# Kernel tuning notes

Measured on AMD Instinct MI355X. Metric: run time of the kernel, lower is better.

The kernel has to match this reference:

```python
import math
import jax, jax.numpy as jnp
import numpy as np

N_HEAD = 16
ROPE_BASE = 10000.0


def _rope_tables(T, half, dtype):
    # build_sin_cos(seq_len, dim=head_dim//2): inv freq of length `half`
    pos = jnp.arange(T, dtype=jnp.float32)[:, None]                       # (T,1)
    inv = jnp.exp(jnp.arange(0, 2 * half, 2, dtype=jnp.float32) * (-math.log(ROPE_BASE) / (2 * half)))
    ang = pos * inv                                                        # (T, half)
    return jnp.sin(ang).astype(dtype), jnp.cos(ang).astype(dtype)


def _apply_rope(q, k, sin, cos):
    # q,k: (B,T,H,Dh); sin,cos: (T, Dh//2) -> broadcast over batch and heads
    half = q.shape[-1] // 2
    s = sin[None, :, None, :]
    c = cos[None, :, None, :]
    q1, q2 = q[..., :half], q[..., half:]
    k1, k2 = k[..., :half], k[..., half:]
    q = jnp.concatenate([q1 * c - q2 * s, q2 * c + q1 * s], axis=-1)
    k = jnp.concatenate([k1 * c - k2 * s, k2 * c + k1 * s], axis=-1)
    return q, k


def setup_inputs() -> dict:
    key = jax.random.key(0)
    k1, k2, k3 = jax.random.split(key, 3)
    B, T, C = 2, 2048, 2048
    x = jax.random.normal(k1, (B, T, C), dtype=jnp.float32)
    w_qkv = jax.random.normal(k2, (3 * C, C), dtype=jnp.float32) * (1.0 / math.sqrt(C))
    w_proj = jax.random.normal(k3, (C, C), dtype=jnp.float32) * (1.0 / math.sqrt(C))
    return {"x": x, "w_qkv": w_qkv, "w_proj": w_proj}


def reference(x, w_qkv, w_proj):
    B, T, C = x.shape
    H = N_HEAD
    Dh = C // H
    # fused QKV projection (Linear, no bias): (B,T,3C) -> (B,T,3,H,Dh)
    qkv = jnp.einsum('btc,oc->bto', x, w_qkv).reshape(B, T, 3, H, Dh)
    q, k, v = qkv[:, :, 0], qkv[:, :, 1], qkv[:, :, 2]          # (B,T,H,Dh)
    sin, cos = _rope_tables(T, Dh // 2, x.dtype)
    q, k = _apply_rope(q, k, sin, cos)
    # causal attention, scale 1/sqrt(Dh) (flash default softmax_scale=None)
    scale = 1.0 / math.sqrt(Dh)
    scores = jnp.einsum('bqhd,bkhd->bhqk', q, k) * scale        # (B,H,T,T)
    mask = jnp.tril(jnp.ones((T, T), dtype=bool))
    scores = jnp.where(mask[None, None], scores, jnp.finfo(scores.dtype).min)
    probs = jax.nn.softmax(scores, axis=-1)
    out = jnp.einsum('bhqk,bkhd->bqhd', probs, v)               # (B,T,H,Dh)
    # faithful to original: permute(0,2,1,3) then reshape_as(x)
    out = jnp.transpose(out, (0, 2, 1, 3)).reshape(B, T, C)
    return jnp.einsum('btc,oc->bto', out, w_proj)
```

## Files before the change

### kernel.cpp

```cpp
#include <hip/hip_runtime.h>
#include <hip/hip_bf16.h>

typedef __bf16 bf16_t;
typedef __bf16 bf16x8 __attribute__((ext_vector_type(8)));
typedef __bf16 bf16x4 __attribute__((ext_vector_type(4)));
typedef float f32x4 __attribute__((ext_vector_type(4)));
typedef float f32x16 __attribute__((ext_vector_type(16)));
typedef unsigned u32x4v __attribute__((ext_vector_type(4)));

#define MFMA16(a, b, c) __builtin_amdgcn_mfma_f32_16x16x32_bf16(a, b, c, 0, 0, 0)
#define MFMA32(a, b, c) __builtin_amdgcn_mfma_f32_32x32x16_bf16(a, b, c, 0, 0, 0)

__device__ __forceinline__ void async_copy16(const void* g, void* l) {
  __builtin_amdgcn_global_load_lds(
      (const __attribute__((address_space(1))) void*)g,
      (__attribute__((address_space(3))) void*)l, 16, 0, 0);
}

__device__ __forceinline__ unsigned cvtpk(float lo, float hi) {
  unsigned r;
  asm("v_cvt_pk_bf16_f32 %0, %1, %2" : "=v"(r) : "v"(lo), "v"(hi));
  return r;
}

__global__ void cast_all(const float* __restrict__ x, const float* __restrict__ wqkv,
                         const float* __restrict__ wproj, bf16_t* __restrict__ xb,
                         bf16_t* __restrict__ wqkvb, bf16_t* __restrict__ wprojb) {
  int stride = gridDim.x * blockDim.x;
  for (int i = blockIdx.x * blockDim.x + threadIdx.x; i < 3145728; i += stride) {
    const float* src;
    bf16_t* dst;
    int idx;
    if (i < 1048576) { src = x; dst = xb; idx = i; }
    else if (i < 2621440) { src = wqkv; dst = wqkvb; idx = i - 1048576; }
    else { src = wproj; dst = wprojb; idx = i - 2621440; }
    const float* p = src + (size_t)idx * 8;
    f32x4 a = *(const f32x4*)p;
    f32x4 b = *(const f32x4*)(p + 4);
    bf16x8 o;
    o[0] = (bf16_t)a[0]; o[1] = (bf16_t)a[1]; o[2] = (bf16_t)a[2]; o[3] = (bf16_t)a[3];
    o[4] = (bf16_t)b[0]; o[5] = (bf16_t)b[1]; o[6] = (bf16_t)b[2]; o[7] = (bf16_t)b[3];
    *(bf16x8*)(dst + (size_t)idx * 8) = o;
  }
}

__global__ __launch_bounds__(512, 2) void gemm_qkv(
    const bf16_t* __restrict__ A, const bf16_t* __restrict__ Bw,
    bf16_t* __restrict__ qo, bf16_t* __restrict__ ko,
    int K) {
  __shared__ __align__(16) char lds[131072];
  int tid = threadIdx.x;
  int w = tid >> 6, lane = tid & 63;
  int wm = w & 1, wn = w >> 1;
  int mr = lane & 15, kg = lane >> 4;

  int orig = blockIdx.x;
  int chunk = orig & 7, i = orig >> 3;
  int by = (chunk & 3) * 4 + (i & 3);
  int bx = (chunk >> 2) * 8 + (i >> 2);
  int row0 = by * 256, col0 = bx * 256;

  int lr = tid >> 3, ch = (tid & 7) ^ (lr & 7);
  size_t aoff[4], boff[4];
#pragma unroll
  for (int g = 0; g < 4; ++g) {
    int gr = g * 32 + (lr & 31) + (lr >> 5) * 128;
    aoff[g] = (size_t)(row0 + gr) * K + ch * 8;
  }
#pragma unroll
  for (int p = 0; p < 4; ++p) {
    int gr = (lr >> 4) * 64 + p * 16 + (lr & 15);
    boff[p] = (size_t)(col0 + gr) * K + ch * 8;
  }

  auto stgA = [&](int q, int g, int kt) {
    async_copy16(A + aoff[g] + kt * 64, lds + q * 65536 + g * 8192 + tid * 16);
  };
  auto stgB = [&](int q, int p, int kt) {
    async_copy16(Bw + boff[p] + kt * 64, lds + q * 65536 + 32768 + p * 8192 + tid * 16);
  };

  f32x4 zero = {0.f, 0.f, 0.f, 0.f};
  f32x4 acc[8][4];
#pragma unroll
  for (int mi = 0; mi < 8; ++mi)
#pragma unroll
    for (int ni = 0; ni < 4; ++ni) acc[mi][ni] = zero;

  int nt = K >> 6;

  stgB(0, 0, 0); stgB(0, 1, 0); stgB(0, 2, 0); stgB(0, 3, 0);
  stgA(0, 0, 0); stgA(0, 1, 0); stgA(0, 2, 0); stgA(0, 3, 0);
  asm volatile("s_waitcnt vmcnt(0)" ::: "memory");
  __builtin_amdgcn_sched_barrier(0);
  __builtin_amdgcn_s_barrier();
  __builtin_amdgcn_sched_barrier(0);

#pragma unroll 1
  for (int t = 0; t < nt; ++t) {
    int q = t & 1, qn = q ^ 1;
    int kt = (t + 1 < nt) ? (t + 1) : t;
    const char* Ab = lds + q * 65536;
    const char* Bb = Ab + 32768;
    bf16x8 bf[4][2];

#define QKV_PHASE(MI0, STG, DOWAIT)                                             \
    {                                                                           \
      int r0 = ((MI0) >> 1) * 64 + wm * 32 + mr;                                \
      int r1 = r0 + 16;                                                         \
      bf16x8 a00 = *(const bf16x8*)(Ab + r0 * 128 + ((kg * 16) ^ ((r0 & 7) << 4)));      \
      bf16x8 a01 = *(const bf16x8*)(Ab + r0 * 128 + ((64 + kg * 16) ^ ((r0 & 7) << 4))); \
      bf16x8 a10 = *(const bf16x8*)(Ab + r1 * 128 + ((kg * 16) ^ ((r1 & 7) << 4)));      \
      bf16x8 a11 = *(const bf16x8*)(Ab + r1 * 128 + ((64 + kg * 16) ^ ((r1 & 7) << 4))); \
      STG;                                                                      \
      __builtin_amdgcn_sched_barrier(0);                                        \
      if (DOWAIT) { asm volatile("s_waitcnt vmcnt(4)" ::: "memory"); }          \
      __builtin_amdgcn_s_barrier();                                             \
      asm volatile("s_waitcnt lgkmcnt(0)" ::: "memory");                        \
      __builtin_amdgcn_sched_barrier(0);                                        \
      __builtin_amdgcn_s_setprio(1);                                            \
      _Pragma("unroll")                                                         \
      for (int ni = 0; ni < 4; ++ni) {                                          \
        acc[MI0][ni] = MFMA16(a00, bf[ni][0], acc[MI0][ni]);                    \
        acc[MI0][ni] = MFMA16(a01, bf[ni][1], acc[MI0][ni]);                    \
        acc[(MI0) + 1][ni] = MFMA16(a10, bf[ni][0], acc[(MI0) + 1][ni]);        \
        acc[(MI0) + 1][ni] = MFMA16(a11, bf[ni][1], acc[(MI0) + 1][ni]);        \
      }                                                                         \
      __builtin_amdgcn_s_setprio(0);                                            \
      __builtin_amdgcn_sched_barrier(0);                                        \
      __builtin_amdgcn_s_barrier();                                             \
      __builtin_amdgcn_sched_barrier(0);                                        \
    }

#pragma unroll
    for (int ni = 0; ni < 4; ++ni) {
      int rb = ni * 64 + wn * 16 + mr;
      bf[ni][0] = *(const bf16x8*)(Bb + rb * 128 + ((kg * 16) ^ ((rb & 7) << 4)));
      bf[ni][1] = *(const bf16x8*)(Bb + rb * 128 + ((64 + kg * 16) ^ ((rb & 7) << 4)));
    }
    QKV_PHASE(0, (stgA(qn, 0, kt), stgA(qn, 1, kt), stgB(qn, 0, kt), stgB(qn, 1, kt)), 1)
    QKV_PHASE(2, (stgA(qn, 2, kt), stgA(qn, 3, kt), stgB(qn, 2, kt), stgB(qn, 3, kt)), 0)
    QKV_PHASE(4, (void)0, 0)
    QKV_PHASE(6, (void)0, 0)
#undef QKV_PHASE
  }
  asm volatile("s_waitcnt vmcnt(0)" ::: "memory");
  __syncthreads();

  char* tb = &lds[0];
  int s = col0 >> 11;
  int h0 = (col0 >> 7) & 15;
  int b = row0 >> 11, t0 = row0 & 2047;
#pragma unroll
  for (int mi = 0; mi < 8; ++mi)
#pragma unroll
    for (int ni = 0; ni < 4; ++ni)
#pragma unroll
      for (int jj = 0; jj < 4; ++jj) {
        int rl = wm * 128 + mi * 16 + kg * 4 + jj;
        int cb = (wn * 64 + ni * 16 + mr) * 2;
        *(bf16_t*)(tb + rl * 512 + (cb ^ ((rl & 7) << 4))) = (bf16_t)acc[mi][ni][jj];
      }
  __syncthreads();
  int r = tid >> 1, hs = tid & 1;
  const char* rowb = tb + r * 512;
  int sz = (r & 7) << 4;
  int t = t0 + r;
  bf16_t* dst = (s == 0 ? qo : ko) + ((size_t)((b * 16 + h0 + hs) * 2048 + t)) * 128;
  float tf = (float)t;
  const float cinv = -0.20762050593046014f;
  float postm = (s == 0) ? 0.12751744f : 1.0f;
  bf16x8 vin[16];
#pragma unroll
  for (int m = 0; m < 16; ++m)
    vin[m] = *(const bf16x8*)(rowb + ((hs * 256 + m * 16) ^ sz));
#pragma unroll
  for (int m = 0; m < 8; ++m) {
    bf16x8 o1, o2;
#pragma unroll
    for (int e = 0; e < 8; ++e) {
      float ang = tf * exp2f((float)(m * 8 + e) * cinv);
      float sv = __sinf(ang), cv = __cosf(ang);
      float x1 = (float)vin[m][e], x2 = (float)vin[m + 8][e];
      o1[e] = (bf16_t)((x1 * cv - x2 * sv) * postm);
      o2[e] = (bf16_t)((x2 * cv + x1 * sv) * postm);
    }
    *(bf16x8*)(dst + m * 8) = o1;
    *(bf16x8*)(dst + 64 + m * 8) = o2;
  }
}

template <int MODE>
__global__ __launch_bounds__(512, 2) void gemm256(
    const bf16_t* __restrict__ A, const bf16_t* __restrict__ Bw, float* __restrict__ C,
    bf16_t* __restrict__ vto, int M, int N, int K, int nby, int colbase) {
  __shared__ __align__(16) char lds[147456];
  int tid = threadIdx.x;
  int w = tid >> 6, lane = tid & 63;
  int wm = w >> 1, wn = w & 1;
  int mr = lane & 15, kg = lane >> 4;

  int nwg = gridDim.x;
  int orig = blockIdx.x;
  int wgid = (orig & 7) * (nwg >> 3) + (orig >> 3);
  int by = wgid % nby, bx = wgid / nby;
  int row0 = by * 256, col0 = colbase + bx * 128;

  size_t aoff[4], boff[2];
#pragma unroll
  for (int it = 0; it < 4; ++it) {
    int c = tid + it * 512;
    int r = c >> 3;
    int chs = (c & 7) ^ (r & 7);
    aoff[it] = (size_t)(row0 + r) * K + chs * 8;
  }
#pragma unroll
  for (int it = 0; it < 2; ++it) {
    int c = tid + it * 512;
    int r = c >> 3;
    int chs = (c & 7) ^ (r & 7);
    boff[it] = (size_t)(col0 - colbase + r) * K + chs * 8;
  }

  auto stageA = [&](int buf, int kt, int half) {
    char* Ad = &lds[buf * 49152];
#pragma unroll
    for (int it = half * 2; it < half * 2 + 2; ++it)
      async_copy16(A + aoff[it] + kt * 64, Ad + (tid + it * 512) * 16);
  };
  auto stageB = [&](int buf, int kt) {
    char* Bd = &lds[buf * 49152 + 32768];
#pragma unroll
    for (int it = 0; it < 2; ++it)
      async_copy16(Bw + boff[it] + kt * 64, Bd + (tid + it * 512) * 16);
  };

  f32x4 zero = {0.f, 0.f, 0.f, 0.f};
  f32x4 acc[4][4];
#pragma unroll
  for (int mi = 0; mi < 4; ++mi)
#pragma unroll
    for (int ni = 0; ni < 4; ++ni) acc[mi][ni] = zero;

  int nt = K >> 6;
  stageA(0, 0, 0); stageA(0, 0, 1); stageB(0, 0);
  stageA(1, 1, 0); stageA(1, 1, 1); stageB(1, 1);
  asm volatile("s_waitcnt vmcnt(6)" ::: "memory");
  __builtin_amdgcn_sched_barrier(0);
  __builtin_amdgcn_s_barrier();
  __builtin_amdgcn_sched_barrier(0);

#pragma unroll 1
  for (int t = 0; t < nt; ++t) {
    int cur = t % 3;
    int nxt = (t + 2) % 3;
    int kt2 = (t + 2 < nt) ? (t + 2) : t;
    const char* Ab = &lds[cur * 49152];
    const char* Bb = &lds[cur * 49152 + 32768];
    bf16x8 af[4][2], bfr[4][2];
#pragma unroll
    for (int mi = 0; mi < 4; ++mi) {
      int row = wm * 64 + mi * 16 + mr;
      const char* rb = Ab + row * 128;
      int sz = (row & 7) << 4;
      af[mi][0] = *(const bf16x8*)(rb + ((kg * 16) ^ sz));
      af[mi][1] = *(const bf16x8*)(rb + ((64 + kg * 16) ^ sz));
    }
#pragma unroll
    for (int ni = 0; ni < 4; ++ni) {
      int row = wn * 64 + ni * 16 + mr;
      const char* rb = Bb + row * 128;
      int sz = (row & 7) << 4;
      bfr[ni][0] = *(const bf16x8*)(rb + ((kg * 16) ^ sz));
      bfr[ni][1] = *(const bf16x8*)(rb + ((64 + kg * 16) ^ sz));
    }
    stageA(nxt, kt2, 0);
    __builtin_amdgcn_s_setprio(1);
#pragma unroll
    for (int mi = 0; mi < 4; ++mi) {
      acc[mi][0] = MFMA16(af[mi][0], bfr[0][0], acc[mi][0]);
      acc[mi][0] = MFMA16(af[mi][1], bfr[0][1], acc[mi][0]);
    }
    __builtin_amdgcn_s_setprio(0);
    stageA(nxt, kt2, 1);
    __builtin_amdgcn_s_setprio(1);
#pragma unroll
    for (int mi = 0; mi < 4; ++mi) {
      acc[mi][1] = MFMA16(af[mi][0], bfr[1][0], acc[mi][1]);
      acc[mi][1] = MFMA16(af[mi][1], bfr[1][1], acc[mi][1]);
    }
    __builtin_amdgcn_s_setprio(0);
    stageB(nxt, kt2);
    __builtin_amdgcn_s_setprio(1);
#pragma unroll
    for (int mi = 0; mi < 4; ++mi) {
      acc[mi][2] = MFMA16(af[mi][0], bfr[2][0], acc[mi][2]);
      acc[mi][2] = MFMA16(af[mi][1], bfr[2][1], acc[mi][2]);
      acc[mi][3] = MFMA16(af[mi][0], bfr[3][0], acc[mi][3]);
      acc[mi][3] = MFMA16(af[mi][1], bfr[3][1], acc[mi][3]);
    }
    __builtin_amdgcn_s_setprio(0);
    asm volatile("s_waitcnt vmcnt(6)" ::: "memory");
    __builtin_amdgcn_sched_barrier(0);
    __builtin_amdgcn_s_barrier();
    __builtin_amdgcn_sched_barrier(0);
  }
  asm volatile("s_waitcnt vmcnt(0)" ::: "memory");
  __syncthreads();

  if (MODE == 0) {
#pragma unroll
    for (int mi = 0; mi < 4; ++mi)
#pragma unroll
      for (int ni = 0; ni < 4; ++ni)
#pragma unroll
        for (int jj = 0; jj < 4; ++jj) {
          int row = row0 + wm * 64 + mi * 16 + kg * 4 + jj;
          int col = col0 + wn * 64 + ni * 16 + mr;
          C[(size_t)row * N + col] = acc[mi][ni][jj];
        }
  } else {
    char* tb = &lds[0];
    int h = (col0 >> 7) & 15;
    int b = row0 >> 11, t0 = row0 & 2047;
#pragma unroll
    for (int mi = 0; mi < 4; ++mi)
#pragma unroll
      for (int ni = 0; ni < 4; ++ni)
#pragma unroll
        for (int jj = 0; jj < 4; ++jj) {
          int rloc = wm * 64 + mi * 16 + kg * 4 + jj;
          int cloc = wn * 64 + ni * 16 + mr;
          *(bf16_t*)(tb + cloc * 512 + ((rloc * 2) ^ ((cloc & 7) << 4))) =
              (bf16_t)acc[mi][ni][jj];
        }
    __syncthreads();
    int d = tid >> 2, qt = tid & 3;
    const char* rowb = tb + d * 512;
    int sz = (d & 7) << 4;
    bf16_t* dst = vto + ((size_t)((b * 16 + h) * 128 + d)) * 2048 + t0 + qt * 64;
#pragma unroll
    for (int m2 = 0; m2 < 8; ++m2)
      *(bf16x8*)(dst + m2 * 8) = *(const bf16x8*)(rowb + ((qt * 128 + m2 * 16) ^ sz));
  }
}

__global__ __launch_bounds__(256, 2) void attn_kernel(
    const bf16_t* __restrict__ qg, const bf16_t* __restrict__ kgl,
    const bf16_t* __restrict__ vtg, bf16_t* __restrict__ og) {
  __shared__ __align__(16) bf16_t Ks[2][64 * 128];
  __shared__ __align__(16) bf16_t Vs[2][128 * 64];
  const int T = 2048;
  int tid = threadIdx.x;
  int w = tid >> 6, lane = tid & 63;
  int l31 = lane & 31, hi = lane >> 5;

  int L = blockIdx.x;
  int halfg = L >> 8;
  int Lr = L & 255;
  int role = (Lr & 7) * 32 + (Lr >> 3);
  int bx = role & 7, bh = role >> 3;
  int qb = halfg ? bx : (15 - bx);

  const bf16_t* Q = qg + (size_t)bh * T * 128;
  const bf16_t* K = kgl + (size_t)bh * T * 128;
  const bf16_t* Vt = vtg + (size_t)bh * 128 * T;

  int sb = tid * 16;
  int krl = sb >> 8;
  int kc = (sb & 255) ^ (krl << 4);
  size_t ksrc = (size_t)krl * 128 + (kc >> 1);
  int vdl = sb >> 7;
  int vc = (sb & 127) ^ ((vdl & 7) << 4);
  size_t vsrc = (size_t)vdl * 2048 + (vc >> 1);

  auto stage = [&](int buf, int kb) {
#pragma unroll
    for (int it = 0; it < 4; ++it)
      async_copy16(K + (size_t)(kb + it * 16) * 128 + ksrc, &Ks[buf][it * 2048 + tid * 8]);
#pragma unroll
    for (int it = 0; it < 4; ++it)
      async_copy16(Vt + (size_t)it * 65536 + kb + vsrc, &Vs[buf][it * 2048 + tid * 8]);
  };

  int b = bh >> 4, h = bh & 15;
  f32x16 zero16 = {0.f};
  int swzK = (l31 & 15) << 4;
  int swzV = (l31 & 7) << 4;

  int qw0 = qb * 128 + w * 32;
  int tq = qw0 + l31;
  const bf16_t* qrow = Q + (size_t)tq * 128 + hi * 8;
  bf16x8 qf[8];
#pragma unroll
  for (int dc = 0; dc < 8; ++dc) qf[dc] = *(const bf16x8*)(qrow + dc * 16);

  f32x16 acc[4];
#pragma unroll
  for (int dt = 0; dt < 4; ++dt) acc[dt] = zero16;
  float mrun = -1e30f, lpart = 0.f;

  int nj = 2 * qb + 2;
  stage(0, 0);
  stage(1, 64);
#pragma unroll 1
  for (int j = 0; j < nj; ++j) {
    int cur = j & 1;
    if (j + 1 < nj) {
      asm volatile("s_waitcnt vmcnt(8)" ::: "memory");
    } else {
      asm volatile("s_waitcnt vmcnt(0)" ::: "memory");
    }
    __builtin_amdgcn_sched_barrier(0);
    __syncthreads();
    int kb = j * 64;
    if (kb <= qw0) {
      const char* KsB = (const char*)&Ks[cur][0];
      const char* VsB = (const char*)&Vs[cur][0];
      f32x16 s0 = zero16, s1 = zero16;
      __builtin_amdgcn_s_setprio(1);
#pragma unroll
      for (int dc = 0; dc < 8; ++dc) {
        int cb = dc * 32 + hi * 16;
        bf16x8 k0 = *(const bf16x8*)(KsB + l31 * 256 + (cb ^ swzK));
        bf16x8 k1 = *(const bf16x8*)(KsB + (32 + l31) * 256 + (cb ^ swzK));
        s0 = MFMA32(k0, qf[dc], s0);
        s1 = MFMA32(k1, qf[dc], s1);
      }
      __builtin_amdgcn_s_setprio(0);
      float p0[16], p1[16];
      float lmax = -3e38f;
      bool diag = (kb + 63 > qw0);
#pragma unroll
      for (int r = 0; r < 16; ++r) {
        int kk = (r & 3) + 8 * (r >> 2) + 4 * hi;
        float v0 = s0[r], v1 = s1[r];
        if (diag) {
          if (kb + kk > tq) v0 = -1e30f;
          if (kb + 32 + kk > tq) v1 = -1e30f;
        }
        p0[r] = v0; p1[r] = v1;
        lmax = fmaxf(lmax, fmaxf(v0, v1));
      }
      bool ok = (lmax <= mrun + 8.0f);
      if (!__all(ok)) {
        float tmax = fmaxf(lmax, __shfl_xor(lmax, 32, 64));
        float mn = fmaxf(mrun, tmax);
        float corr = __builtin_amdgcn_exp2f(mrun - mn);
        mrun = mn;
        lpart *= corr;
#pragma unroll
        for (int dt = 0; dt < 4; ++dt)
#pragma unroll
          for (int r = 0; r < 16; ++r) acc[dt][r] *= corr;
      }
#pragma unroll
      for (int r = 0; r < 16; ++r) {
        float e0 = __builtin_amdgcn_exp2f(p0[r] - mrun);
        float e1 = __builtin_amdgcn_exp2f(p1[r] - mrun);
        p0[r] = e0; p1[r] = e1;
        lpart += e0 + e1;
      }
      bf16x8 pa0, pa1, pa2, pa3;
#define BUILD_PA(dst, P, B0)                                         \
      { unsigned a0 = cvtpk(P[(B0) + 0], P[(B0) + 1]);               \
        unsigned a1 = cvtpk(P[(B0) + 2], P[(B0) + 3]);               \
        unsigned b0 = cvtpk(P[(B0) + 4], P[(B0) + 5]);               \
        unsigned b1 = cvtpk(P[(B0) + 6], P[(B0) + 7]);               \
        unsigned xa0 = __shfl_xor(a0, 32, 64);                       \
        unsigned xa1 = __shfl_xor(a1, 32, 64);                       \
        unsigned xb0 = __shfl_xor(b0, 32, 64);                       \
        unsigned xb1 = __shfl_xor(b1, 32, 64);                       \
        u32x4v fw;                                                   \
        fw[0] = hi ? xb0 : a0; fw[1] = hi ? xb1 : a1;                \
        fw[2] = hi ? b0 : xa0; fw[3] = hi ? b1 : xa1;                \
        dst = __builtin_bit_cast(bf16x8, fw); }
      BUILD_PA(pa0, p0, 0)
      BUILD_PA(pa1, p0, 8)
      BUILD_PA(pa2, p1, 0)
      BUILD_PA(pa3, p1, 8)
#undef BUILD_PA
      __builtin_amdgcn_s_setprio(1);
#pragma unroll
      for (int dt = 0; dt < 4; ++dt) {
        const char* vrow = VsB + (dt * 32 + l31) * 128;
        bf16x8 v0 = *(const bf16x8*)(vrow + ((hi * 16) ^ swzV));
        bf16x8 v1 = *(const bf16x8*)(vrow + ((32 + hi * 16) ^ swzV));
        bf16x8 v2 = *(const bf16x8*)(vrow + ((64 + hi * 16) ^ swzV));
        bf16x8 v3 = *(const bf16x8*)(vrow + ((96 + hi * 16) ^ swzV));
        acc[dt] = MFMA32(v0, pa0, acc[dt]);
        acc[dt] = MFMA32(v1, pa1, acc[dt]);
        acc[dt] = MFMA32(v2, pa2, acc[dt]);
        acc[dt] = MFMA32(v3, pa3, acc[dt]);
      }
      __builtin_amdgcn_s_setprio(0);
    }
    __syncthreads();
    if (j + 2 < nj) stage(cur, (j + 2) * 64);
  }
  float l = lpart + __shfl_xor(lpart, 32, 64);
  float invl = 1.0f / l;
  size_t orow_idx = (size_t)b * 2048 + h * 128 + (tq >> 4);
  bf16_t* orow = og + orow_idx * 2048 + (tq & 15) * 128;
#pragma unroll
  for (int dt = 0; dt < 4; ++dt)
#pragma unroll
    for (int g = 0; g < 4; ++g) {
      bf16x4 v4;
#pragma unroll
      for (int e = 0; e < 4; ++e) v4[e] = (bf16_t)(acc[dt][4 * g + e] * invl);
      *(bf16x4*)(orow + dt * 32 + 8 * g + 4 * hi) = v4;
    }
}

extern "C" void kernel_launch(void* const* d_in, const int* in_sizes, int n_in,
                              void* d_out, int out_size, void* d_ws, size_t ws_size,
                              hipStream_t stream) {
  const float* x = (const float*)d_in[0];
  const float* wqkv = (const float*)d_in[1];
  const float* wproj = (const float*)d_in[2];
  float* out = (float*)d_out;
  char* ws = (char*)d_ws;

  const size_t OFF_WQKV = 16777216;
  const size_t OFF_WPROJ = 41943040;
  const size_t OFF_Q = 50331648;
  const size_t OFF_K = 67108864;
  const size_t OFF_VT = 83886080;

  bf16_t* xb = (bf16_t*)(ws);
  bf16_t* wqkvb = (bf16_t*)(ws + OFF_WQKV);
  bf16_t* wprojb = (bf16_t*)(ws + OFF_WPROJ);
  bf16_t* g_q = (bf16_t*)(ws + OFF_Q);
  bf16_t* g_k = (bf16_t*)(ws + OFF_K);
  bf16_t* g_vt = (bf16_t*)(ws + OFF_VT);
  bf16_t* g_att = (bf16_t*)(ws);

  cast_all<<<4096, 256, 0, stream>>>(x, wqkv, wproj, xb, wqkvb, wprojb);
  gemm_qkv<<<256, 512, 0, stream>>>(xb, wqkvb, g_q, g_k, 2048);
  gemm256<1><<<256, 512, 0, stream>>>(xb, wqkvb + (size_t)4096 * 2048, nullptr, g_vt,
                                      4096, 2048, 2048, 16, 4096);
  attn_kernel<<<512, 256, 0, stream>>>(g_q, g_k, g_vt, g_att);
  gemm256<0><<<256, 512, 0, stream>>>(g_att, wprojb, out, nullptr, 4096, 2048, 2048, 16, 0);
}
```

Measured before the change: 243.3 us.

## Software-pipeline QK^T of next key tile with softmax of current tile

Splits K and V staging into separate async loads and triple-buffers K in LDS. Each iteration now computes the QK^T MFMAs for tile j+1 while the softmax and PV work of tile j runs, so matrix-core and VALU/transcendental work can overlap instead of running back to back. In exchange, the per-warp causal skip of fully masked tiles is removed, the prologue gets extra waits, register pressure grows by the extra score accumulators, and LDS use per block rises.

```diff
diff --git a/kernel.cpp b/kernel.cpp
--- a/kernel.cpp
+++ b/kernel.cpp
@@ -348,7 +348,7 @@
 __global__ __launch_bounds__(256, 2) void attn_kernel(
     const bf16_t* __restrict__ qg, const bf16_t* __restrict__ kgl,
     const bf16_t* __restrict__ vtg, bf16_t* __restrict__ og) {
-  __shared__ __align__(16) bf16_t Ks[2][64 * 128];
+  __shared__ __align__(16) bf16_t Ks[3][64 * 128];
   __shared__ __align__(16) bf16_t Vs[2][128 * 64];
   const int T = 2048;
   int tid = threadIdx.x;
@@ -374,10 +374,12 @@
   int vc = (sb & 127) ^ ((vdl & 7) << 4);
   size_t vsrc = (size_t)vdl * 2048 + (vc >> 1);
 
-  auto stage = [&](int buf, int kb) {
+  auto stageK = [&](int buf, int kb) {
 #pragma unroll
     for (int it = 0; it < 4; ++it)
       async_copy16(K + (size_t)(kb + it * 16) * 128 + ksrc, &Ks[buf][it * 2048 + tid * 8]);
+  };
+  auto stageV = [&](int buf, int kb) {
 #pragma unroll
     for (int it = 0; it < 4; ++it)
       async_copy16(Vt + (size_t)it * 65536 + kb + vsrc, &Vs[buf][it * 2048 + tid * 8]);
@@ -400,86 +402,101 @@
   for (int dt = 0; dt < 4; ++dt) acc[dt] = zero16;
   float mrun = -1e30f, lpart = 0.f;
 
+#define QK_TILE(BUF, S0, S1)                                                   \
+  { const char* KsB_ = (const char*)&Ks[BUF][0];                               \
+    _Pragma("unroll")                                                          \
+    for (int dc = 0; dc < 8; ++dc) {                                           \
+      int cb = dc * 32 + hi * 16;                                              \
+      bf16x8 k0_ = *(const bf16x8*)(KsB_ + l31 * 256 + (cb ^ swzK));           \
+      bf16x8 k1_ = *(const bf16x8*)(KsB_ + (32 + l31) * 256 + (cb ^ swzK));    \
+      S0 = MFMA32(k0_, qf[dc], S0);                                            \
+      S1 = MFMA32(k1_, qf[dc], S1);                                            \
+    } }
+
   int nj = 2 * qb + 2;
-  stage(0, 0);
-  stage(1, 64);
+  stageK(0, 0);
+  stageV(0, 0);
+  stageK(1, 64);
+  stageV(1, 64);
+  if (nj > 2) {
+    stageK(2, 128);
+    asm volatile("s_waitcnt vmcnt(16)" ::: "memory");
+  } else {
+    asm volatile("s_waitcnt vmcnt(12)" ::: "memory");
+  }
+  __builtin_amdgcn_sched_barrier(0);
+  __syncthreads();
+  f32x16 sc0 = zero16, sc1 = zero16;
+  QK_TILE(0, sc0, sc1)
+
 #pragma unroll 1
   for (int j = 0; j < nj; ++j) {
-    int cur = j & 1;
-    if (j + 1 < nj) {
+    int kb = j * 64;
+    if (j + 2 < nj) {
       asm volatile("s_waitcnt vmcnt(8)" ::: "memory");
     } else {
       asm volatile("s_waitcnt vmcnt(0)" ::: "memory");
     }
     __builtin_amdgcn_sched_barrier(0);
     __syncthreads();
-    int kb = j * 64;
-    if (kb <= qw0) {
-      const char* KsB = (const char*)&Ks[cur][0];
-      const char* VsB = (const char*)&Vs[cur][0];
-      f32x16 s0 = zero16, s1 = zero16;
-      __builtin_amdgcn_s_setprio(1);
-#pragma unroll
-      for (int dc = 0; dc < 8; ++dc) {
-        int cb = dc * 32 + hi * 16;
-        bf16x8 k0 = *(const bf16x8*)(KsB + l31 * 256 + (cb ^ swzK));
-        bf16x8 k1 = *(const bf16x8*)(KsB + (32 + l31) * 256 + (cb ^ swzK));
-        s0 = MFMA32(k0, qf[dc], s0);
-        s1 = MFMA32(k1, qf[dc], s1);
+    f32x16 sn0 = zero16, sn1 = zero16;
+    if (j + 1 < nj) {
+      QK_TILE((j + 1) % 3, sn0, sn1)
+    }
+    float p0[16], p1[16];
+    float lmax = -3e38f;
+    bool diag = (kb + 63 > qw0);
+#pragma unroll
+    for (int r = 0; r < 16; ++r) {
+      int kk = (r & 3) + 8 * (r >> 2) + 4 * hi;
+      float v0 = sc0[r], v1 = sc1[r];
+      if (diag) {
+        if (kb + kk > tq) v0 = -1e30f;
+        if (kb + 32 + kk > tq) v1 = -1e30f;
       }
-      __builtin_amdgcn_s_setprio(0);
-      float p0[16], p1[16];
-      float lmax = -3e38f;
-      bool diag = (kb + 63 > qw0);
-#pragma unroll
-      for (int r = 0; r < 16; ++r) {
-        int kk = (r & 3) + 8 * (r >> 2) + 4 * hi;
-        float v0 = s0[r], v1 = s1[r];
-        if (diag) {
-          if (kb + kk > tq) v0 = -1e30f;
-          if (kb + 32 + kk > tq) v1 = -1e30f;
-        }
-        p0[r] = v0; p1[r] = v1;
-        lmax = fmaxf(lmax, fmaxf(v0, v1));
-      }
-      bool ok = (lmax <= mrun + 8.0f);
-      if (!__all(ok)) {
-        float tmax = fmaxf(lmax, __shfl_xor(lmax, 32, 64));
-        float mn = fmaxf(mrun, tmax);
-        float corr = __builtin_amdgcn_exp2f(mrun - mn);
-        mrun = mn;
-        lpart *= corr;
-#pragma unroll
-        for (int dt = 0; dt < 4; ++dt)
-#pragma unroll
-          for (int r = 0; r < 16; ++r) acc[dt][r] *= corr;
-      }
-#pragma unroll
-      for (int r = 0; r < 16; ++r) {
-        float e0 = __builtin_amdgcn_exp2f(p0[r] - mrun);
-        float e1 = __builtin_amdgcn_exp2f(p1[r] - mrun);
-        p0[r] = e0; p1[r] = e1;
-        lpart += e0 + e1;
-      }
-      bf16x8 pa0, pa1, pa2, pa3;
+      p0[r] = v0; p1[r] = v1;
+      lmax = fmaxf(lmax, fmaxf(v0, v1));
+    }
+    bool ok = (lmax <= mrun + 8.0f);
+    if (!__all(ok)) {
+      float tmax = fmaxf(lmax, __shfl_xor(lmax, 32, 64));
+      float mn = fmaxf(mrun, tmax);
+      float corr = __builtin_amdgcn_exp2f(mrun - mn);
+      mrun = mn;
+      lpart *= corr;
+#pragma unroll
+      for (int dt = 0; dt < 4; ++dt)
+#pragma unroll
+        for (int r = 0; r < 16; ++r) acc[dt][r] *= corr;
+    }
+#pragma unroll
+    for (int r = 0; r < 16; ++r) {
+      float e0 = __builtin_amdgcn_exp2f(p0[r] - mrun);
+      float e1 = __builtin_amdgcn_exp2f(p1[r] - mrun);
+      p0[r] = e0; p1[r] = e1;
+      lpart += e0 + e1;
+    }
+    bf16x8 pa0, pa1, pa2, pa3;
 #define BUILD_PA(dst, P, B0)                                         \
-      { unsigned a0 = cvtpk(P[(B0) + 0], P[(B0) + 1]);               \
-        unsigned a1 = cvtpk(P[(B0) + 2], P[(B0) + 3]);               \
-        unsigned b0 = cvtpk(P[(B0) + 4], P[(B0) + 5]);               \
-        unsigned b1 = cvtpk(P[(B0) + 6], P[(B0) + 7]);               \
-        unsigned xa0 = __shfl_xor(a0, 32, 64);                       \
-        unsigned xa1 = __shfl_xor(a1, 32, 64);                       \
-        unsigned xb0 = __shfl_xor(b0, 32, 64);                       \
-        unsigned xb1 = __shfl_xor(b1, 32, 64);                       \
-        u32x4v fw;                                                   \
-        fw[0] = hi ? xb0 : a0; fw[1] = hi ? xb1 : a1;                \
-        fw[2] = hi ? b0 : xa0; fw[3] = hi ? b1 : xa1;                \
-        dst = __builtin_bit_cast(bf16x8, fw); }
-      BUILD_PA(pa0, p0, 0)
-      BUILD_PA(pa1, p0, 8)
-      BUILD_PA(pa2, p1, 0)
-      BUILD_PA(pa3, p1, 8)
+    { unsigned a0 = cvtpk(P[(B0) + 0], P[(B0) + 1]);                 \
+      unsigned a1 = cvtpk(P[(B0) + 2], P[(B0) + 3]);                 \
+      unsigned b0 = cvtpk(P[(B0) + 4], P[(B0) + 5]);                 \
+      unsigned b1 = cvtpk(P[(B0) + 6], P[(B0) + 7]);                 \
+      unsigned xa0 = __shfl_xor(a0, 32, 64);                         \
+      unsigned xa1 = __shfl_xor(a1, 32, 64);                         \
+      unsigned xb0 = __shfl_xor(b0, 32, 64);                         \
+      unsigned xb1 = __shfl_xor(b1, 32, 64);                         \
+      u32x4v fw;                                                     \
+      fw[0] = hi ? xb0 : a0; fw[1] = hi ? xb1 : a1;                  \
+      fw[2] = hi ? b0 : xa0; fw[3] = hi ? b1 : xa1;                  \
+      dst = __builtin_bit_cast(bf16x8, fw); }
+    BUILD_PA(pa0, p0, 0)
+    BUILD_PA(pa1, p0, 8)
+    BUILD_PA(pa2, p1, 0)
+    BUILD_PA(pa3, p1, 8)
 #undef BUILD_PA
+    {
+      const char* VsB = (const char*)&Vs[j & 1][0];
       __builtin_amdgcn_s_setprio(1);
 #pragma unroll
       for (int dt = 0; dt < 4; ++dt) {
@@ -496,8 +513,12 @@
       __builtin_amdgcn_s_setprio(0);
     }
     __syncthreads();
-    if (j + 2 < nj) stage(cur, (j + 2) * 64);
-  }
+    if (j + 2 < nj) stageV(j & 1, (j + 2) * 64);
+    if (j + 3 < nj) stageK((j + 3) % 3, (j + 3) * 64);
+    sc0 = sn0;
+    sc1 = sn1;
+  }
+#undef QK_TILE
   float l = lpart + __shfl_xor(lpart, 32, 64);
   float invl = 1.0f / l;
   size_t orow_idx = (size_t)b * 2048 + h * 128 + (tq >> 4);
```

Result: no change. 242.0 us, median of 2 (-0.5%).
